# Kernel tuning notes

Measured on AMD Instinct MI355X. Metric: run time of the kernel, lower is better.

Reference implementation:

```python
import jax, jax.numpy as jnp
import numpy as np

B, S, H, A = 64, 512, 512, 512
NC, V, ED, NF, L = 4, 1000, 128, 6, 2


def _pos_encoding(seq_len, d, base=10000.0):
    pos = jnp.arange(seq_len, dtype=jnp.float32)[:, None]
    i = jnp.arange(0, d, 2, dtype=jnp.float32)[None, :]
    ang = pos / jnp.power(base, i / d)
    pe = jnp.zeros((seq_len, d), dtype=jnp.float32)
    pe = pe.at[:, 0::2].set(jnp.sin(ang))
    pe = pe.at[:, 1::2].set(jnp.cos(ang))
    return pe  # [S, H]


def setup_inputs() -> dict:
    key = jax.random.key(0)
    ks = jax.random.split(key, 20)
    inp = {}
    inp['cate_x'] = jax.random.randint(ks[0], (B, S, NC), 0, V)
    inp['cont_x'] = jax.random.normal(ks[1], (B, S, NF), dtype=jnp.float32)
    inp['mask'] = jnp.ones((B, S), dtype=jnp.int64)
    inp['targets'] = jax.random.uniform(ks[2], (B, S), dtype=jnp.float32)
    s = 0.02
    inp['emb'] = jax.random.normal(ks[3], (NC, V, ED), dtype=jnp.float32) * s
    inp['W_cont'] = jax.random.normal(ks[4], (NF, H), dtype=jnp.float32) * s
    inp['b_cont'] = jnp.zeros((H,), dtype=jnp.float32)
    inp['W_comb'] = jax.random.normal(ks[5], (NC * ED + H, H), dtype=jnp.float32) * s
    inp['b_comb'] = jnp.zeros((H,), dtype=jnp.float32)
    inp['Wq'] = jax.random.normal(ks[6], (H, A), dtype=jnp.float32) * s
    inp['Wk'] = jax.random.normal(ks[7], (H, A), dtype=jnp.float32) * s
    inp['Wv'] = jax.random.normal(ks[8], (H, A), dtype=jnp.float32) * s
    inp['Wi'] = jax.random.normal(ks[9], (L, 3 * A, A), dtype=jnp.float32) * s
    inp['Wh'] = jax.random.normal(ks[10], (L, 3 * A, A), dtype=jnp.float32) * s
    inp['bi'] = jnp.zeros((L, 3 * A), dtype=jnp.float32)
    inp['bh'] = jnp.zeros((L, 3 * A), dtype=jnp.float32)
    inp['W_fin'] = jax.random.normal(ks[11], (A, 1), dtype=jnp.float32) * s
    inp['b_fin'] = jnp.zeros((1,), dtype=jnp.float32)
    return inp


def _gru_layer(x_seq, Wi, Wh, bi, bh):
    # x_seq: [S, B, A]; PyTorch gate order: r, z, n
    def step(h, x):
        gi = x @ Wi.T + bi            # [B, 3A]
        gh = h @ Wh.T + bh
        ir, iz, inn = jnp.split(gi, 3, axis=-1)
        hr, hz, hn = jnp.split(gh, 3, axis=-1)
        r = jax.nn.sigmoid(ir + hr)
        zg = jax.nn.sigmoid(iz + hz)
        n = jnp.tanh(inn + r * hn)
        h_new = (1.0 - zg) * n + zg * h
        return h_new, h_new
    h0 = jnp.zeros((x_seq.shape[1], Wh.shape[1]), dtype=x_seq.dtype)
    _, hs = jax.lax.scan(step, h0, x_seq)
    return hs  # [S, B, A]


def reference(cate_x, cont_x, mask, targets, emb, W_cont, b_cont, W_comb, b_comb,
              Wq, Wk, Wv, Wi, Wh, bi, bh, W_fin, b_fin):
    # Entire embedding: per-feature categorical lookup + continuous projection
    ce = emb[jnp.arange(NC), cate_x]                 # [B, S, NC, ED]
    ce = ce.reshape(B, S, NC * ED)                   # [B, S, 512]
    cp = cont_x @ W_cont + b_cont                    # [B, S, H]
    x = jnp.concatenate([ce, cp], axis=-1) @ W_comb + b_comb  # [B, S, H]
    x = x + _pos_encoding(S, H)[None]
    Q = x @ Wq
    K = x @ Wk
    Vv = x @ Wv
    scores = jnp.einsum('bqd,bkd->bqk', Q, K) / jnp.sqrt(jnp.float32(A))
    scores = jax.nn.softmax(scores, axis=1)          # softmax over QUERY axis (dim=1), as in source
    z = jnp.einsum('bqk,bkd->bqd', scores, Vv)       # [B, S, A]
    h = jnp.transpose(z, (1, 0, 2))                  # [S, B, A]
    for l in range(L):
        h = _gru_layer(h, Wi[l], Wh[l], bi[l], bh[l])
    hs = jnp.transpose(h, (1, 0, 2))                 # [B, S, A]
    out = jax.nn.sigmoid(hs @ W_fin + b_fin)         # [B, S, 1]
    return out.squeeze(-1)
```

## Files before the change

kernel.cpp:

```cpp
#include <hip/hip_runtime.h>
#include <hip/hip_bf16.h>
#include <math.h>

typedef unsigned short u16;
typedef unsigned int   u32;
typedef unsigned long long u64;
typedef __attribute__((ext_vector_type(8))) short short8;
typedef __attribute__((ext_vector_type(4))) float float4v;

#define BB 64
#define SS 512

__device__ __forceinline__ u16 f2b(float f) {
    u32 x = __float_as_uint(f);
    u32 r = (x + 0x7fffu + ((x >> 16) & 1u)) >> 16;
    return (u16)r;
}
__device__ __forceinline__ float b2f(u32 lo16) { return __uint_as_float(lo16 << 16); }
__device__ __forceinline__ float b2fh(u32 v)   { return __uint_as_float(v & 0xffff0000u); }

__global__ __launch_bounds__(256) void zero_kernel(float* __restrict__ p, int n) {
    int i = blockIdx.x * 256 + threadIdx.x;
    if (i < n) p[i] = 0.f;
}

__global__ __launch_bounds__(256) void pe_kernel(float* __restrict__ pe) {
    int s = blockIdx.x, j = threadIdx.x;
    float ang = (float)s * powf(10000.0f, -(2.0f * (float)j) / 512.0f);
    pe[s * 512 + 2 * j]     = sinf(ang);
    pe[s * 512 + 2 * j + 1] = cosf(ang);
}

__global__ __launch_bounds__(256) void transp_w(const float* __restrict__ in,
                                                u16* __restrict__ out, int R, int C) {
    __shared__ float t[64][65];
    int r0 = blockIdx.x * 64, c0 = blockIdx.y * 64;
    int tid = threadIdx.x;
    int lr = tid >> 4, lc4 = (tid & 15) * 4;
#pragma unroll
    for (int i = 0; i < 4; i++) {
        int r = lr + i * 16;
        float4 v = *(const float4*)(in + (long)(r0 + r) * C + c0 + lc4);
        t[r][lc4] = v.x; t[r][lc4 + 1] = v.y; t[r][lc4 + 2] = v.z; t[r][lc4 + 3] = v.w;
    }
    __syncthreads();
#pragma unroll
    for (int i = 0; i < 4; i++) {
        int c = lr + i * 16;
        u32 lo = (u32)f2b(t[lc4][c])     | ((u32)f2b(t[lc4 + 1][c]) << 16);
        u32 hi = (u32)f2b(t[lc4 + 2][c]) | ((u32)f2b(t[lc4 + 3][c]) << 16);
        uint2 pk; pk.x = lo; pk.y = hi;
        *(uint2*)(out + (long)(c0 + c) * R + r0 + lc4) = pk;
    }
}

__global__ __launch_bounds__(256) void cvt_bf16(const float* __restrict__ in,
                                                u16* __restrict__ out, long n) {
    long i = (long)blockIdx.x * 256 + threadIdx.x;
    if (i < n) out[i] = f2b(in[i]);
}

__global__ __launch_bounds__(256) void transp_b(const u16* __restrict__ in,
                                                u16* __restrict__ out,
                                                int R, int C, int ldin,
                                                long sbin, long sb, long sc) {
    __shared__ u32 t[64][65];
    int bz = blockIdx.z;
    in += (long)bz * sbin;
    int r0 = blockIdx.x * 64, c0 = blockIdx.y * 64;
    int tid = threadIdx.x;
    int lr = tid >> 4, lc4 = (tid & 15) * 4;
#pragma unroll
    for (int i = 0; i < 4; i++) {
        int r = lr + i * 16;
        uint2 v = *(const uint2*)(in + (long)(r0 + r) * ldin + c0 + lc4);
        t[r][lc4] = v.x & 0xffffu; t[r][lc4 + 1] = v.x >> 16;
        t[r][lc4 + 2] = v.y & 0xffffu; t[r][lc4 + 3] = v.y >> 16;
    }
    __syncthreads();
#pragma unroll
    for (int i = 0; i < 4; i++) {
        int c = lr + i * 16;
        uint2 pk;
        pk.x = t[lc4][c] | (t[lc4 + 1][c] << 16);
        pk.y = t[lc4 + 2][c] | (t[lc4 + 3][c] << 16);
        *(uint2*)(out + (long)bz * sb + (long)(c0 + c) * sc + r0 + lc4) = pk;
    }
}

__global__ __launch_bounds__(256) void embed_kernel(
    const int* __restrict__ cate, const float* __restrict__ cont,
    const float* __restrict__ emb, const float* __restrict__ Wc,
    const float* __restrict__ bc, u16* __restrict__ xc, int gbase)
{
    long bs = (long)gbase + blockIdx.x;
    long r  = blockIdx.x;
    __shared__ float cf[6];
    if (threadIdx.x < 6) cf[threadIdx.x] = cont[bs * 6 + threadIdx.x];
    __syncthreads();
    for (int h = threadIdx.x; h < 1024; h += 256) {
        float v;
        if (h < 512) {
            int c = h >> 7, e = h & 127;
            int idx = cate[bs * 4 + c];
            v = emb[((long)c * 1000 + idx) * 128 + e];
        } else {
            int hh = h - 512;
            v = bc[hh];
#pragma unroll
            for (int f = 0; f < 6; f++) v += cf[f] * Wc[f * 512 + hh];
        }
        xc[r * 1024 + h] = f2b(v);
    }
}

__global__ __launch_bounds__(256) void gemm_nt(
    const u16* __restrict__ A, const u16* __restrict__ B, void* __restrict__ Cv,
    int K, int lda, int ldb, int ldc,
    long sA, long sB, long sC,
    const float* __restrict__ bias, const float* __restrict__ pe,
    float alpha, int outBf16)
{
    __shared__ u16 As[128][40];
    __shared__ u16 Bs[128][40];

    A += (long)blockIdx.z * sA;
    B += (long)blockIdx.z * sB;
    int m0 = blockIdx.y * 128, n0 = blockIdx.x * 128;
    int tid = threadIdx.x;
    int lane = tid & 63, wid = tid >> 6;
    int wm = (wid >> 1) * 64, wn = (wid & 1) * 64;
    int mrow = lane & 15, q8 = (lane >> 4) * 8;

    float4v acc[4][4];
#pragma unroll
    for (int i = 0; i < 4; i++)
#pragma unroll
        for (int j = 0; j < 4; j++) { float4v z = {0.f, 0.f, 0.f, 0.f}; acc[i][j] = z; }

    for (int k0 = 0; k0 < K; k0 += 32) {
        {
            int r = tid >> 2, sg = tid & 3;
            *(short8*)&As[r][sg * 8] = *(const short8*)(A + (long)(m0 + r) * lda + k0 + sg * 8);
            *(short8*)&Bs[r][sg * 8] = *(const short8*)(B + (long)(n0 + r) * ldb + k0 + sg * 8);
            r = (tid + 256) >> 2;
            *(short8*)&As[r][sg * 8] = *(const short8*)(A + (long)(m0 + r) * lda + k0 + sg * 8);
            *(short8*)&Bs[r][sg * 8] = *(const short8*)(B + (long)(n0 + r) * ldb + k0 + sg * 8);
        }
        __syncthreads();
        short8 af[4], bfr[4];
#pragma unroll
        for (int t = 0; t < 4; t++) {
            af[t]  = *(const short8*)&As[wm + t * 16 + mrow][q8];
            bfr[t] = *(const short8*)&Bs[wn + t * 16 + mrow][q8];
        }
#pragma unroll
        for (int i = 0; i < 4; i++)
#pragma unroll
            for (int j = 0; j < 4; j++)
                acc[i][j] = __builtin_amdgcn_mfma_f32_16x16x32_bf16(af[i], bfr[j], acc[i][j], 0, 0, 0);
        __syncthreads();
    }

    int col = lane & 15, quad = lane >> 4;
    u16*  Cb = (u16*)Cv  + (outBf16 ? (long)blockIdx.z * sC : 0);
    float* Cf = (float*)Cv + (outBf16 ? 0 : (long)blockIdx.z * sC);
#pragma unroll
    for (int i = 0; i < 4; i++)
#pragma unroll
        for (int j = 0; j < 4; j++) {
#pragma unroll
            for (int rr = 0; rr < 4; rr++) {
                int gm = m0 + wm + i * 16 + quad * 4 + rr;
                int gn = n0 + wn + j * 16 + col;
                float v = acc[i][j][rr] * alpha;
                if (bias) v += bias[gn];
                if (pe)   v += pe[(long)(gm & 511) * 512 + gn];
                if (outBf16) Cb[(long)gm * ldc + gn] = f2b(v);
                else         Cf[(long)gm * ldc + gn] = v;
            }
        }
}

__global__ __launch_bounds__(64) void softmax_q(const float* __restrict__ S,
                                                u16* __restrict__ P) {
    int b = blockIdx.x;
    int k = blockIdx.y * 64 + threadIdx.x;
    const float* p = S + (long)b * 262144 + k;
    u16* o = P + (long)b * 262144 + k;
    float m = -1e30f;
    for (int q = 0; q < 512; q++) m = fmaxf(m, p[(long)q * 512]);
    float sum = 0.f;
    for (int q = 0; q < 512; q++) sum += expf(p[(long)q * 512] - m);
    float inv = 1.f / sum;
    for (int q = 0; q < 512; q++) o[(long)q * 512] = f2b(expf(p[(long)q * 512] - m) * inv);
}

__global__ __launch_bounds__(256, 1) void gru_mfma(
    const float* __restrict__ gi,
    const u16*  __restrict__ WhB,
    const float* __restrict__ bh_l,
    u16* __restrict__ seq_out,
    u64* __restrict__ hx,
    int s0, int layer)
{
    __shared__ u16 hlds[16 * 512];
    __shared__ float pre[3 * 16 * 34];
    __shared__ float hprev[8 * 32];

    int blk = blockIdx.x;
    int bg  = blk & 7;
    int us  = blk >> 3;
    int tid = threadIdx.x;
    int lane = tid & 63, wid = tid >> 6;

    int fb = (tid >> 4) & 7, up = tid & 15;
    int u0 = up << 1;
    int ug = (us << 5) + u0;
    float2 bhr = *(const float2*)(bh_l + ug);
    float2 bhz = *(const float2*)(bh_l + 512 + ug);
    float2 bhn = *(const float2*)(bh_l + 1024 + ug);

    int t0 = (wid < 2) ? (wid << 1) : (wid + 2);
    int nt2 = (wid < 2);
    int bq = lane & 15, kq = (lane >> 4) << 3;
    char* hbase = (char*)hlds + (bq << 10);
    int swz = (bq & 7) << 4;

    short8 br0[16], br1[16];
    {
        int r_0 = (t0 << 4) + bq;
        long grow0 = (long)((r_0 >> 5) << 9) + (us << 5) + (r_0 & 31);
        const u16* wp0 = WhB + grow0 * 512 + kq;
#pragma unroll
        for (int ks = 0; ks < 16; ks++) br0[ks] = *(const short8*)(wp0 + ks * 32);
        if (nt2) {
            int r_1 = r_0 + 16;
            long grow1 = (long)((r_1 >> 5) << 9) + (us << 5) + (r_1 & 31);
            const u16* wp1 = WhB + grow1 * 512 + kq;
#pragma unroll
            for (int ks = 0; ks < 16; ks++) br1[ks] = *(const short8*)(wp1 + ks * 32);
        } else {
#pragma unroll
            for (int ks = 0; ks < 16; ks++) br1[ks] = br0[ks];
        }
    }

    for (int sl = 0; sl < 128; sl++) {
        int s = s0 + sl;

        float2 gir = {0.f, 0.f}, giz = {0.f, 0.f}, gin = {0.f, 0.f};
        if (tid < 128) {
            const float* g = gi + ((long)sl * 64 + (bg << 3) + fb) * 1536 + ug;
            gir = *(const float2*)g;
            giz = *(const float2*)(g + 512);
            gin = *(const float2*)(g + 1024);
        }

        if (s == 0) {
            u32* hz = (u32*)hlds;
            for (int i = tid; i < 4096; i += 256) hz[i] = 0;
        } else {
            u32 exp_tag = (u32)(layer * 512 + s);
            const u64* src = hx + ((long)(exp_tag & 1) << 14) + ((long)bg << 11) + tid;
            u32 need = 0xffu;
            int guard = 0;
            while (need) {
                u64 v[8];
#pragma unroll
                for (int j = 0; j < 8; j++)
                    v[j] = __hip_atomic_load(src + (j << 8), __ATOMIC_RELAXED, __HIP_MEMORY_SCOPE_AGENT);
#pragma unroll
                for (int j = 0; j < 8; j++) {
                    if ((need & (1u << j)) && (u32)(v[j] >> 32) == exp_tag) {
                        int i = tid + (j << 8);
                        int b = i & 7, pr = i >> 3;
                        *(u32*)((char*)hlds + ((b << 10) + ((pr << 2) ^ (b << 4)))) = (u32)v[j];
                        need &= ~(1u << j);
                    }
                }
                if (need) {
                    __builtin_amdgcn_s_sleep(1);
                    if (++guard > (1 << 12)) break;
                }
            }
        }
        __syncthreads();

        if (sl == 0 && tid < 128) {
            int pr = (us << 4) + up;
            u32 pk = *(u32*)((char*)hlds + ((fb << 10) + ((pr << 2) ^ (fb << 4))));
            hprev[(fb << 5) + u0]     = b2f(pk & 0xffffu);
            hprev[(fb << 5) + u0 + 1] = b2fh(pk);
        }

        {
            float4v acc0 = {0.f, 0.f, 0.f, 0.f}, acc1 = {0.f, 0.f, 0.f, 0.f};
#pragma unroll
            for (int ks = 0; ks < 16; ks++) {
                int k2 = ((ks << 5) + kq) << 1;
                short8 a = *(const short8*)(hbase + (k2 ^ swz));
                acc0 = __builtin_amdgcn_mfma_f32_16x16x32_bf16(a, br0[ks], acc0, 0, 0, 0);
                if (nt2)
                    acc1 = __builtin_amdgcn_mfma_f32_16x16x32_bf16(a, br1[ks], acc1, 0, 0, 0);
            }
            int gq = lane >> 4;
            int g0 = t0 >> 1;
            int uu0 = ((t0 << 4) + (lane & 15)) & 31;
#pragma unroll
            for (int rr = 0; rr < 4; rr++) {
                int b = (gq << 2) + rr;
                pre[(g0 * 16 + b) * 34 + uu0] = acc0[rr];
                if (nt2) {
                    int t1 = t0 + 1;
                    int uu1 = ((t1 << 4) + (lane & 15)) & 31;
                    pre[((t1 >> 1) * 16 + b) * 34 + uu1] = acc1[rr];
                }
            }
        }
        __syncthreads();

        if (tid < 128) {
            float2 sr = *(const float2*)&pre[(0 * 16 + fb) * 34 + u0];
            float2 sz = *(const float2*)&pre[(1 * 16 + fb) * 34 + u0];
            float2 sn = *(const float2*)&pre[(2 * 16 + fb) * 34 + u0];
            float r0v = 1.f / (1.f + expf(-(gir.x + sr.x + bhr.x)));
            float r1v = 1.f / (1.f + expf(-(gir.y + sr.y + bhr.y)));
            float z0v = 1.f / (1.f + expf(-(giz.x + sz.x + bhz.x)));
            float z1v = 1.f / (1.f + expf(-(giz.y + sz.y + bhz.y)));
            float n0v = tanhf(gin.x + r0v * (sn.x + bhn.x));
            float n1v = tanhf(gin.y + r1v * (sn.y + bhn.y));
            float hp0 = hprev[(fb << 5) + u0];
            float hp1 = hprev[(fb << 5) + u0 + 1];
            float hn0 = (1.f - z0v) * n0v + z0v * hp0;
            float hn1 = (1.f - z1v) * n1v + z1v * hp1;
            hprev[(fb << 5) + u0]     = hn0;
            hprev[(fb << 5) + u0 + 1] = hn1;
            u16 q0 = f2b(hn0), q1 = f2b(hn1);
            u32 pk = ((u32)q1 << 16) | (u32)q0;
            u32 wt = (u32)(layer * 512 + s + 1);
            u64 pv = ((u64)wt << 32) | (u64)pk;
            int slot = (((us << 4) + up) << 3) + fb;
            u64* dst = hx + ((long)(wt & 1) << 14) + ((long)bg << 11) + slot;
            __hip_atomic_store(dst, pv, __ATOMIC_RELAXED, __HIP_MEMORY_SCOPE_AGENT);
            *(u32*)(seq_out + ((long)s * 64 + (bg << 3) + fb) * 512 + ug) = pk;
        }
    }
}

__global__ __launch_bounds__(256) void final_kernel(
    const u16* __restrict__ h2, const float* __restrict__ Wf,
    const float* __restrict__ bfin, float* __restrict__ out)
{
    int w = blockIdx.x * 4 + (threadIdx.x >> 6);
    int lane = threadIdx.x & 63;
    const u16* row = h2 + (long)w * 512;
    uint4 hv = *(const uint4*)(row + lane * 8);
    float4 w0 = *(const float4*)(Wf + lane * 8);
    float4 w1 = *(const float4*)(Wf + lane * 8 + 4);
    float sum = b2f(hv.x & 0xffffu) * w0.x + b2fh(hv.x) * w0.y
              + b2f(hv.y & 0xffffu) * w0.z + b2fh(hv.y) * w0.w
              + b2f(hv.z & 0xffffu) * w1.x + b2fh(hv.z) * w1.y
              + b2f(hv.w & 0xffffu) * w1.z + b2fh(hv.w) * w1.w;
#pragma unroll
    for (int off = 32; off > 0; off >>= 1) sum += __shfl_down(sum, off, 64);
    if (lane == 0) {
        int s = w >> 6, b = w & 63;
        out[(long)b * 512 + s] = 1.f / (1.f + expf(-(sum + bfin[0])));
    }
}

extern "C" void kernel_launch(void* const* d_in, const int* in_sizes, int n_in,
                              void* d_out, int out_size, void* d_ws, size_t ws_size,
                              hipStream_t stream) {
    const int*   cate  = (const int*)  d_in[0];
    const float* cont  = (const float*)d_in[1];
    const float* emb   = (const float*)d_in[4];
    const float* Wc    = (const float*)d_in[5];
    const float* bc    = (const float*)d_in[6];
    const float* Wcomb = (const float*)d_in[7];
    const float* bcomb = (const float*)d_in[8];
    const float* Wq    = (const float*)d_in[9];
    const float* Wk    = (const float*)d_in[10];
    const float* Wv    = (const float*)d_in[11];
    const float* Wi    = (const float*)d_in[12];
    const float* Wh    = (const float*)d_in[13];
    const float* bi    = (const float*)d_in[14];
    const float* bh    = (const float*)d_in[15];
    const float* Wf    = (const float*)d_in[16];
    const float* bfin  = (const float*)d_in[17];
    float* out = (float*)d_out;
    char* ws = (char*)d_ws;

    u16*   zp    = (u16*)(ws + 0);
    u16*   h2bf  = (u16*)(ws + 0);
    u16*   h1bf  = (u16*)(ws + 33554432);
    float* gi    = (float*)(ws + 67108864);
    u16*   xbf   = (u16*)(ws + 67108864);
    u16*   QKV   = (u16*)(ws + 117440512);
    u16*   Vt    = (u16*)(ws + 130023424);
    float* Sg    = (float*)(ws + 134217728);
    u64*   hx    = (u64*)  (ws + 134217728);
    u16*   Pg    = (u16*)(ws + 142606336);
    u16*   zT    = (u16*)(ws + 146800640);
    u16*   xc    = (u16*)(ws + 150994944);
    u16*   WcombT= (u16*)(ws + 159383552);
    u16*   WqT   = (u16*)(ws + 160432128);
    u16*   WkT   = (u16*)(ws + 160956416);
    u16*   WvT   = (u16*)(ws + 161480704);
    u16*   WiB   = (u16*)(ws + 162004992);
    float* pe    = (float*)(ws + 165150720);
    u16*   WhB   = (u16*)(ws + 166199296);

    transp_w<<<dim3(16, 8), 256, 0, stream>>>(Wcomb, WcombT, 1024, 512);
    transp_w<<<dim3(8, 8),  256, 0, stream>>>(Wq, WqT, 512, 512);
    transp_w<<<dim3(8, 8),  256, 0, stream>>>(Wk, WkT, 512, 512);
    transp_w<<<dim3(8, 8),  256, 0, stream>>>(Wv, WvT, 512, 512);
    cvt_bf16<<<6144, 256, 0, stream>>>(Wi, WiB, 2L * 1536 * 512);
    cvt_bf16<<<6144, 256, 0, stream>>>(Wh, WhB, 2L * 1536 * 512);
    pe_kernel<<<512, 256, 0, stream>>>(pe);

    for (int g = 0; g < 8; g++) {
        embed_kernel<<<4096, 256, 0, stream>>>(cate, cont, emb, Wc, bc, xc, g * 4096);
        gemm_nt<<<dim3(4, 32, 1), 256, 0, stream>>>(
            xc, WcombT, xbf + (long)g * 4096 * 512, 1024, 1024, 1024, 512,
            0, 0, 0, bcomb, pe, 1.f, 1);
    }

    for (int g = 0; g < 8; g++) {
        const u16* xg = xbf + (long)g * 8 * 512 * 512;
        gemm_nt<<<dim3(12, 32, 1), 256, 0, stream>>>(xg, WqT, QKV, 512,
                                                     512, 512, 1536,
                                                     0, 0, 0, nullptr, nullptr, 1.f, 1);
        transp_b<<<dim3(8, 8, 8), 256, 0, stream>>>(QKV + 1024, Vt, 512, 512, 1536,
                                                    (long)512 * 1536, 262144, 512);
        gemm_nt<<<dim3(4, 4, 8), 256, 0, stream>>>(QKV, QKV + 512, Sg, 512,
                                                   1536, 1536, 512,
                                                   (long)512 * 1536, (long)512 * 1536, 262144,
                                                   nullptr, nullptr,
                                                   0.04419417382415922f, 0);
        softmax_q<<<dim3(8, 8), 64, 0, stream>>>(Sg, Pg);
        gemm_nt<<<dim3(4, 4, 8), 256, 0, stream>>>(Vt, Pg, zT, 512, 512, 512, 512,
                                                   262144, 262144, 262144, nullptr, nullptr,
                                                   1.f, 1);
        transp_b<<<dim3(8, 8, 8), 256, 0, stream>>>(zT, zp + (long)g * 8 * 512,
                                                    512, 512, 512, 262144, 512, 32768);
    }

    zero_kernel<<<256, 256, 0, stream>>>((float*)hx, 65536);
    for (int l = 0; l < 2; l++) {
        const u16* Aseq = (l == 0) ? zp : h1bf;
        u16* seqOut = (l == 0) ? h1bf : h2bf;
        const u16* WiL = WiB + (long)l * 1536 * 512;
        const u16* WhL = WhB + (long)l * 1536 * 512;
        const float* biL = bi + (long)l * 1536;
        const float* bhL = bh + (long)l * 1536;
        for (int seg = 0; seg < 4; seg++) {
            gemm_nt<<<dim3(12, 64, 1), 256, 0, stream>>>(
                Aseq + (long)seg * 128 * 64 * 512, WiL, gi, 512, 512, 512, 1536,
                0, 0, 0, biL, nullptr, 1.f, 0);
            const float* giP = gi;
            u16* soP = seqOut;
            int s0v = seg * 128;
            int lv = l;
            void* args[] = { (void*)&giP, (void*)&WhL, (void*)&bhL, (void*)&soP,
                             (void*)&hx, (void*)&s0v, (void*)&lv };
            hipLaunchCooperativeKernel((void*)gru_mfma, dim3(128), dim3(256),
                                       args, 0, stream);
        }
    }

    final_kernel<<<8192, 256, 0, stream>>>(h2bf, Wf, bfin, out);
}
```

Before: 5.693 ms.

## Fuse both GRU layers into one cooperative kernel with wavefront pipelining

Layer 0 and layer 1 now run in the same cooperative launch: 128 blocks per layer, and layer-1 blocks wait on per-block step flags published by layer 0. Layer 1 computes its input projection in-kernel with a second MFMA pass over h1 staged in LDS, so the separate input GEMM for that layer goes away. Blocks grow to 512 threads, one 16-row tile per wave. This overlaps the two serial recurrences and removes launches, at the cost of flag spin-waits, more LDS and registers per block, and 256 co-resident blocks.

```diff
diff --git a/kernel.cpp b/kernel.cpp
--- a/kernel.cpp
+++ b/kernel.cpp
@@ -196,84 +196,104 @@
     for (int q = 0; q < 512; q++) o[(long)q * 512] = f2b(expf(p[(long)q * 512] - m) * inv);
 }
 
-__global__ __launch_bounds__(256, 1) void gru_mfma(
-    const float* __restrict__ gi,
-    const u16*  __restrict__ WhB,
-    const float* __restrict__ bh_l,
-    u16* __restrict__ seq_out,
-    u64* __restrict__ hx,
-    int s0, int layer)
+__global__ __launch_bounds__(512, 1) void gru_fused(
+    const float* __restrict__ gi0,
+    const u16* __restrict__ Wh0, const u16* __restrict__ Wh1,
+    const u16* __restrict__ Wi1,
+    const float* __restrict__ bh0, const float* __restrict__ bh1,
+    const float* __restrict__ bi1,
+    u16* __restrict__ h1bf, u16* __restrict__ h2bf,
+    u64* __restrict__ hx, int s0)
 {
     __shared__ u16 hlds[16 * 512];
-    __shared__ float pre[3 * 16 * 34];
+    __shared__ u16 xlds[16 * 512];
+    __shared__ float pre[6 * 16 * 34];
     __shared__ float hprev[8 * 32];
 
     int blk = blockIdx.x;
+    int lyr = blk >> 7;
     int bg  = blk & 7;
-    int us  = blk >> 3;
+    int us  = (blk >> 3) & 15;
     int tid = threadIdx.x;
     int lane = tid & 63, wid = tid >> 6;
+
+    u64* hxL   = hx + (long)lyr * 32768;
+    u32* flags = (u32*)(hx + 65536);
 
     int fb = (tid >> 4) & 7, up = tid & 15;
     int u0 = up << 1;
     int ug = (us << 5) + u0;
+    const float* bh_l = lyr ? bh1 : bh0;
     float2 bhr = *(const float2*)(bh_l + ug);
     float2 bhz = *(const float2*)(bh_l + 512 + ug);
     float2 bhn = *(const float2*)(bh_l + 1024 + ug);
-
-    int t0 = (wid < 2) ? (wid << 1) : (wid + 2);
-    int nt2 = (wid < 2);
+    float2 bir = {0.f, 0.f}, biz = {0.f, 0.f}, bin = {0.f, 0.f};
+    if (lyr) {
+        bir = *(const float2*)(bi1 + ug);
+        biz = *(const float2*)(bi1 + 512 + ug);
+        bin = *(const float2*)(bi1 + 1024 + ug);
+    }
+
+    int t = wid;
     int bq = lane & 15, kq = (lane >> 4) << 3;
     char* hbase = (char*)hlds + (bq << 10);
+    char* xbase = (char*)xlds + (bq << 10);
     int swz = (bq & 7) << 4;
 
-    short8 br0[16], br1[16];
+    short8 brh[16], bri[16];
+    if (t < 6) {
+        int r_ = (t << 4) + bq;
+        long grow = (long)((r_ >> 5) << 9) + (us << 5) + (r_ & 31);
+        const u16* whp = (lyr ? Wh1 : Wh0) + grow * 512 + kq;
+#pragma unroll
+        for (int ks = 0; ks < 16; ks++) brh[ks] = *(const short8*)(whp + ks * 32);
+        if (lyr) {
+            const u16* wip = Wi1 + grow * 512 + kq;
+#pragma unroll
+            for (int ks = 0; ks < 16; ks++) bri[ks] = *(const short8*)(wip + ks * 32);
+        }
+    }
+
     {
-        int r_0 = (t0 << 4) + bq;
-        long grow0 = (long)((r_0 >> 5) << 9) + (us << 5) + (r_0 & 31);
-        const u16* wp0 = WhB + grow0 * 512 + kq;
-#pragma unroll
-        for (int ks = 0; ks < 16; ks++) br0[ks] = *(const short8*)(wp0 + ks * 32);
-        if (nt2) {
-            int r_1 = r_0 + 16;
-            long grow1 = (long)((r_1 >> 5) << 9) + (us << 5) + (r_1 & 31);
-            const u16* wp1 = WhB + grow1 * 512 + kq;
-#pragma unroll
-            for (int ks = 0; ks < 16; ks++) br1[ks] = *(const short8*)(wp1 + ks * 32);
-        } else {
-#pragma unroll
-            for (int ks = 0; ks < 16; ks++) br1[ks] = br0[ks];
-        }
-    }
+        u32* hz = (u32*)hlds;
+        u32* xz = (u32*)xlds;
+#pragma unroll
+        for (int i = 0; i < 8; i++) { hz[tid + i * 512] = 0; xz[tid + i * 512] = 0; }
+    }
+    __syncthreads();
 
     for (int sl = 0; sl < 128; sl++) {
         int s = s0 + sl;
 
-        float2 gir = {0.f, 0.f}, giz = {0.f, 0.f}, gin = {0.f, 0.f};
-        if (tid < 128) {
-            const float* g = gi + ((long)sl * 64 + (bg << 3) + fb) * 1536 + ug;
-            gir = *(const float2*)g;
-            giz = *(const float2*)(g + 512);
-            gin = *(const float2*)(g + 1024);
-        }
-
-        if (s == 0) {
-            u32* hz = (u32*)hlds;
-            for (int i = tid; i < 4096; i += 256) hz[i] = 0;
-        } else {
-            u32 exp_tag = (u32)(layer * 512 + s);
-            const u64* src = hx + ((long)(exp_tag & 1) << 14) + ((long)bg << 11) + tid;
-            u32 need = 0xffu;
+        if (lyr) {
+            u32 needv = (u32)(s + 1);
+            u32* fp = flags + (bg << 4) + (lane & 15);
+            int guard = 0;
+            for (;;) {
+                u32 f = __hip_atomic_load(fp, __ATOMIC_ACQUIRE, __HIP_MEMORY_SCOPE_AGENT);
+                if (__all((int)(f - needv) >= 0)) break;
+                __builtin_amdgcn_s_sleep(1);
+                if (++guard > (1 << 13)) break;
+            }
+            int b = tid >> 6, k8 = tid & 63;
+            short8 xv = *(const short8*)(h1bf + ((long)s * 64 + (bg << 3) + b) * 512 + (k8 << 3));
+            *(short8*)((char*)xlds + ((b << 10) + ((k8 << 4) ^ (b << 4)))) = xv;
+        }
+
+        if (s > 0) {
+            u32 exp_tag = (u32)(lyr * 512 + s);
+            const u64* src = hxL + ((long)(exp_tag & 1) << 14) + ((long)bg << 11) + tid;
+            u32 need = 0xfu;
             int guard = 0;
             while (need) {
-                u64 v[8];
-#pragma unroll
-                for (int j = 0; j < 8; j++)
-                    v[j] = __hip_atomic_load(src + (j << 8), __ATOMIC_RELAXED, __HIP_MEMORY_SCOPE_AGENT);
-#pragma unroll
-                for (int j = 0; j < 8; j++) {
+                u64 v[4];
+#pragma unroll
+                for (int j = 0; j < 4; j++)
+                    v[j] = __hip_atomic_load(src + (j << 9), __ATOMIC_RELAXED, __HIP_MEMORY_SCOPE_AGENT);
+#pragma unroll
+                for (int j = 0; j < 4; j++) {
                     if ((need & (1u << j)) && (u32)(v[j] >> 32) == exp_tag) {
-                        int i = tid + (j << 8);
+                        int i = tid + (j << 9);
                         int b = i & 7, pr = i >> 3;
                         *(u32*)((char*)hlds + ((b << 10) + ((pr << 2) ^ (b << 4)))) = (u32)v[j];
                         need &= ~(1u << j);
@@ -287,6 +307,18 @@
         }
         __syncthreads();
 
+        if (!lyr && tid == 0)
+            __hip_atomic_store(flags + (bg << 4) + us, (u32)(s0 + sl),
+                               __ATOMIC_RELAXED, __HIP_MEMORY_SCOPE_AGENT);
+
+        float2 g_r = {0.f, 0.f}, g_z = {0.f, 0.f}, g_n = {0.f, 0.f};
+        if (!lyr && tid < 128) {
+            const float* g = gi0 + ((long)sl * 64 + (bg << 3) + fb) * 1536 + ug;
+            g_r = *(const float2*)g;
+            g_z = *(const float2*)(g + 512);
+            g_n = *(const float2*)(g + 1024);
+        }
+
         if (sl == 0 && tid < 128) {
             int pr = (us << 4) + up;
             u32 pk = *(u32*)((char*)hlds + ((fb << 10) + ((pr << 2) ^ (fb << 4))));
@@ -294,27 +326,33 @@
             hprev[(fb << 5) + u0 + 1] = b2fh(pk);
         }
 
-        {
-            float4v acc0 = {0.f, 0.f, 0.f, 0.f}, acc1 = {0.f, 0.f, 0.f, 0.f};
+        if (t < 6) {
+            float4v acc = {0.f, 0.f, 0.f, 0.f};
 #pragma unroll
             for (int ks = 0; ks < 16; ks++) {
                 int k2 = ((ks << 5) + kq) << 1;
                 short8 a = *(const short8*)(hbase + (k2 ^ swz));
-                acc0 = __builtin_amdgcn_mfma_f32_16x16x32_bf16(a, br0[ks], acc0, 0, 0, 0);
-                if (nt2)
-                    acc1 = __builtin_amdgcn_mfma_f32_16x16x32_bf16(a, br1[ks], acc1, 0, 0, 0);
+                acc = __builtin_amdgcn_mfma_f32_16x16x32_bf16(a, brh[ks], acc, 0, 0, 0);
             }
             int gq = lane >> 4;
-            int g0 = t0 >> 1;
-            int uu0 = ((t0 << 4) + (lane & 15)) & 31;
+            int uu = ((t << 4) + (lane & 15)) & 31;
 #pragma unroll
             for (int rr = 0; rr < 4; rr++) {
                 int b = (gq << 2) + rr;
-                pre[(g0 * 16 + b) * 34 + uu0] = acc0[rr];
-                if (nt2) {
-                    int t1 = t0 + 1;
-                    int uu1 = ((t1 << 4) + (lane & 15)) & 31;
-                    pre[((t1 >> 1) * 16 + b) * 34 + uu1] = acc1[rr];
+                pre[((t >> 1) * 16 + b) * 34 + uu] = acc[rr];
+            }
+            if (lyr) {
+                float4v accx = {0.f, 0.f, 0.f, 0.f};
+#pragma unroll
+                for (int ks = 0; ks < 16; ks++) {
+                    int k2 = ((ks << 5) + kq) << 1;
+                    short8 a = *(const short8*)(xbase + (k2 ^ swz));
+                    accx = __builtin_amdgcn_mfma_f32_16x16x32_bf16(a, bri[ks], accx, 0, 0, 0);
+                }
+#pragma unroll
+                for (int rr = 0; rr < 4; rr++) {
+                    int b = (gq << 2) + rr;
+                    pre[((3 + (t >> 1)) * 16 + b) * 34 + uu] = accx[rr];
                 }
             }
         }
@@ -324,12 +362,20 @@
             float2 sr = *(const float2*)&pre[(0 * 16 + fb) * 34 + u0];
             float2 sz = *(const float2*)&pre[(1 * 16 + fb) * 34 + u0];
             float2 sn = *(const float2*)&pre[(2 * 16 + fb) * 34 + u0];
-            float r0v = 1.f / (1.f + expf(-(gir.x + sr.x + bhr.x)));
-            float r1v = 1.f / (1.f + expf(-(gir.y + sr.y + bhr.y)));
-            float z0v = 1.f / (1.f + expf(-(giz.x + sz.x + bhz.x)));
-            float z1v = 1.f / (1.f + expf(-(giz.y + sz.y + bhz.y)));
-            float n0v = tanhf(gin.x + r0v * (sn.x + bhn.x));
-            float n1v = tanhf(gin.y + r1v * (sn.y + bhn.y));
+            if (lyr) {
+                float2 xr = *(const float2*)&pre[(3 * 16 + fb) * 34 + u0];
+                float2 xz = *(const float2*)&pre[(4 * 16 + fb) * 34 + u0];
+                float2 xn = *(const float2*)&pre[(5 * 16 + fb) * 34 + u0];
+                g_r.x = xr.x + bir.x; g_r.y = xr.y + bir.y;
+                g_z.x = xz.x + biz.x; g_z.y = xz.y + biz.y;
+                g_n.x = xn.x + bin.x; g_n.y = xn.y + bin.y;
+            }
+            float r0v = 1.f / (1.f + expf(-(g_r.x + sr.x + bhr.x)));
+            float r1v = 1.f / (1.f + expf(-(g_r.y + sr.y + bhr.y)));
+            float z0v = 1.f / (1.f + expf(-(g_z.x + sz.x + bhz.x)));
+            float z1v = 1.f / (1.f + expf(-(g_z.y + sz.y + bhz.y)));
+            float n0v = tanhf(g_n.x + r0v * (sn.x + bhn.x));
+            float n1v = tanhf(g_n.y + r1v * (sn.y + bhn.y));
             float hp0 = hprev[(fb << 5) + u0];
             float hp1 = hprev[(fb << 5) + u0 + 1];
             float hn0 = (1.f - z0v) * n0v + z0v * hp0;
@@ -338,13 +384,21 @@
             hprev[(fb << 5) + u0 + 1] = hn1;
             u16 q0 = f2b(hn0), q1 = f2b(hn1);
             u32 pk = ((u32)q1 << 16) | (u32)q0;
-            u32 wt = (u32)(layer * 512 + s + 1);
+            u32 wt = (u32)(lyr * 512 + s + 1);
             u64 pv = ((u64)wt << 32) | (u64)pk;
             int slot = (((us << 4) + up) << 3) + fb;
-            u64* dst = hx + ((long)(wt & 1) << 14) + ((long)bg << 11) + slot;
+            u64* dst = hxL + ((long)(wt & 1) << 14) + ((long)bg << 11) + slot;
             __hip_atomic_store(dst, pv, __ATOMIC_RELAXED, __HIP_MEMORY_SCOPE_AGENT);
-            *(u32*)(seq_out + ((long)s * 64 + (bg << 3) + fb) * 512 + ug) = pk;
-        }
+            u16* so = lyr ? h2bf : h1bf;
+            *(u32*)(so + ((long)s * 64 + (bg << 3) + fb) * 512 + ug) = pk;
+        }
+    }
+
+    if (!lyr) {
+        __syncthreads();
+        if (tid == 0)
+            __hip_atomic_store(flags + (bg << 4) + us, (u32)(s0 + 128),
+                               __ATOMIC_RELAXED, __HIP_MEMORY_SCOPE_AGENT);
     }
 }
 
@@ -393,17 +447,17 @@
     char* ws = (char*)d_ws;
 
     u16*   zp    = (u16*)(ws + 0);
-    u16*   h2bf  = (u16*)(ws + 0);
     u16*   h1bf  = (u16*)(ws + 33554432);
     float* gi    = (float*)(ws + 67108864);
     u16*   xbf   = (u16*)(ws + 67108864);
     u16*   QKV   = (u16*)(ws + 117440512);
+    u16*   h2bf  = (u16*)(ws + 117440512);
     u16*   Vt    = (u16*)(ws + 130023424);
     float* Sg    = (float*)(ws + 134217728);
-    u64*   hx    = (u64*)  (ws + 134217728);
     u16*   Pg    = (u16*)(ws + 142606336);
     u16*   zT    = (u16*)(ws + 146800640);
     u16*   xc    = (u16*)(ws + 150994944);
+    u64*   hx    = (u64*)  (ws + 150994944);
     u16*   WcombT= (u16*)(ws + 159383552);
     u16*   WqT   = (u16*)(ws + 160432128);
     u16*   WkT   = (u16*)(ws + 160956416);
@@ -447,27 +501,27 @@
                                                     512, 512, 512, 262144, 512, 32768);
     }
 
-    zero_kernel<<<256, 256, 0, stream>>>((float*)hx, 65536);
-    for (int l = 0; l < 2; l++) {
-        const u16* Aseq = (l == 0) ? zp : h1bf;
-        u16* seqOut = (l == 0) ? h1bf : h2bf;
-        const u16* WiL = WiB + (long)l * 1536 * 512;
-        const u16* WhL = WhB + (long)l * 1536 * 512;
-        const float* biL = bi + (long)l * 1536;
-        const float* bhL = bh + (long)l * 1536;
-        for (int seg = 0; seg < 4; seg++) {
-            gemm_nt<<<dim3(12, 64, 1), 256, 0, stream>>>(
-                Aseq + (long)seg * 128 * 64 * 512, WiL, gi, 512, 512, 512, 1536,
-                0, 0, 0, biL, nullptr, 1.f, 0);
-            const float* giP = gi;
-            u16* soP = seqOut;
-            int s0v = seg * 128;
-            int lv = l;
-            void* args[] = { (void*)&giP, (void*)&WhL, (void*)&bhL, (void*)&soP,
-                             (void*)&hx, (void*)&s0v, (void*)&lv };
-            hipLaunchCooperativeKernel((void*)gru_mfma, dim3(128), dim3(256),
-                                       args, 0, stream);
-        }
+    zero_kernel<<<513, 256, 0, stream>>>((float*)hx, 131328);
+    for (int seg = 0; seg < 4; seg++) {
+        gemm_nt<<<dim3(12, 64, 1), 256, 0, stream>>>(
+            zp + (long)seg * 128 * 64 * 512, WiB, gi, 512, 512, 512, 1536,
+            0, 0, 0, bi, nullptr, 1.f, 0);
+        const float* giP = gi;
+        const u16* wh0 = WhB;
+        const u16* wh1 = WhB + 786432;
+        const u16* wi1 = WiB + 786432;
+        const float* bh0p = bh;
+        const float* bh1p = bh + 1536;
+        const float* bi1p = bi + 1536;
+        u16* h1P = h1bf;
+        u16* h2P = h2bf;
+        u64* hxP = hx;
+        int s0v = seg * 128;
+        void* args[] = { (void*)&giP, (void*)&wh0, (void*)&wh1, (void*)&wi1,
+                         (void*)&bh0p, (void*)&bh1p, (void*)&bi1p,
+                         (void*)&h1P, (void*)&h2P, (void*)&hxP, (void*)&s0v };
+        hipLaunchCooperativeKernel((void*)gru_fused, dim3(256), dim3(512),
+                                   args, 0, stream);
     }
 
     final_kernel<<<8192, 256, 0, stream>>>(h2bf, Wf, bfin, out);
```

Result: slower. 7.258 ms (+27.5%).
